# Kernel optimization log

Hardware: AMD Instinct MI355X
Metric: run time of the kernel (lower is better)

Reference implementation:

```python
import jax, jax.numpy as jnp
import numpy as np
import math

B, S, D, H = 2, 2048, 1024, 16
DK = D // H


def setup_inputs() -> dict:
    key = jax.random.key(0)
    ks = jax.random.split(key, 12)
    scale = 1.0 / math.sqrt(D)
    inp = {
        "query": jax.random.normal(ks[0], (B, S, D), jnp.float32),
        "key": jax.random.normal(ks[1], (B, S, D), jnp.float32),
        "value": jax.random.normal(ks[2], (B, S, D), jnp.float32),
        # causal 0/1 mask, broadcast over heads
        "mask": jnp.broadcast_to(jnp.tril(jnp.ones((S, S), jnp.int32)), (B, 1, S, S)),
        "Wq": jax.random.normal(ks[3], (D, D), jnp.float32) * scale,
        "bq": jnp.zeros((D,), jnp.float32),
        "Wk": jax.random.normal(ks[4], (D, D), jnp.float32) * scale,
        "bk": jnp.zeros((D,), jnp.float32),
        "Wv": jax.random.normal(ks[5], (D, D), jnp.float32) * scale,
        "bv": jnp.zeros((D,), jnp.float32),
        "Wo": jax.random.normal(ks[6], (D, D), jnp.float32) * scale,
        "bo": jnp.zeros((D,), jnp.float32),
    }
    return inp


def _split_heads(x):
    # [B,S,D] -> [B,H,S,DK]
    return x.reshape(B, S, H, DK).transpose(0, 2, 1, 3)


def reference(query, key, value, mask, Wq, bq, Wk, bk, Wv, bv, Wo, bo):
    q = _split_heads(query @ Wq.T + bq)
    k = _split_heads(key @ Wk.T + bk)
    v = _split_heads(value @ Wv.T + bv)
    # scaled dot-product attention with additive mask (mask==0 -> -inf)
    scores = jnp.einsum("bhqd,bhkd->bhqk", q, k) / math.sqrt(DK)
    scores = jnp.where(mask == 0, -jnp.inf, scores)
    w = jax.nn.softmax(scores, axis=-1)
    out = jnp.einsum("bhqk,bhkd->bhqd", w, v)
    out = out.transpose(0, 2, 1, 3).reshape(B, S, D)
    return out @ Wo.T + bo
```

## Files before the change

### kernel.cpp

```cpp
#include <hip/hip_runtime.h>
#include <hip/hip_bf16.h>
#include <math.h>

#define BBATCH 2
#define SSEQ 2048
#define DMODEL 1024
#define NH 16
#define MTOT (BBATCH*SSEQ)

typedef short bfrag __attribute__((ext_vector_type(8)));
typedef float ffrag __attribute__((ext_vector_type(4)));

typedef const __attribute__((address_space(1))) unsigned int* gas_t;
typedef __attribute__((address_space(3))) unsigned int* las_t;

__device__ __forceinline__ void dl16(const void* g, void* l) {
  __builtin_amdgcn_global_load_lds((gas_t)(unsigned long long)g,
                                   (las_t)(unsigned int)(unsigned long long)l,
                                   16, 0, 0);
}

__device__ __forceinline__ void drain_vm() {
  asm volatile("s_waitcnt vmcnt(0)" ::: "memory");
}

__device__ __forceinline__ unsigned short f2bf(float f) {
  union { float f; unsigned u; } v; v.f = f;
  unsigned r = v.u + 0x7fffu + ((v.u >> 16) & 1u);
  return (unsigned short)(r >> 16);
}

__global__ __launch_bounds__(256) void convert_all_kernel(
    const float* __restrict__ q, const float* __restrict__ k, const float* __restrict__ v,
    const float* __restrict__ wq, const float* __restrict__ wk,
    const float* __restrict__ wv, const float* __restrict__ wo,
    unsigned short* __restrict__ dst)
{
  const long NIN = (long)MTOT * DMODEL;
  const long NW  = (long)DMODEL * DMODEL;
  const long total8 = (3 * NIN + 4 * NW) >> 3;
  long i8 = (long)blockIdx.x * blockDim.x + threadIdx.x;
  const long stride = (long)gridDim.x * blockDim.x;
  for (; i8 < total8; i8 += stride) {
    const long i = i8 << 3;
    const float* src; long off;
    if (i < NIN)          { src = q; off = i; }
    else if (i < 2 * NIN) { src = k; off = i - NIN; }
    else if (i < 3 * NIN) { src = v; off = i - 2 * NIN; }
    else {
      const long j = i - 3 * NIN;
      const int wsel = (int)(j >> 20);
      off = j & (NW - 1);
      src = (wsel == 0) ? wq : (wsel == 1) ? wk : (wsel == 2) ? wv : wo;
    }
    const float4 x0 = *(const float4*)(src + off);
    const float4 x1 = *(const float4*)(src + off + 4);
    ushort4 o0, o1;
    o0.x = f2bf(x0.x); o0.y = f2bf(x0.y); o0.z = f2bf(x0.z); o0.w = f2bf(x0.w);
    o1.x = f2bf(x1.x); o1.y = f2bf(x1.y); o1.z = f2bf(x1.z); o1.w = f2bf(x1.w);
    union { ushort4 s[2]; uint4 u; } pk; pk.s[0] = o0; pk.s[1] = o1;
    *(uint4*)(dst + i) = pk.u;
  }
}

struct ProjArgs {
  const unsigned short* X[3];
  const unsigned short* W[3];
  const float* bias[3];
  unsigned short* dst[3];
  float scale[3];
};

__global__ __launch_bounds__(256, 2) void qkv_proj(ProjArgs a)
{
  __shared__ alignas(16) unsigned short As[2][128 * 64];
  __shared__ alignas(16) unsigned short Bs[2][128 * 64];
  const int t = threadIdx.x;
  const int lane = t & 63, w = t >> 6;
  const int quad = lane >> 4, l16 = lane & 15;
  const int m0 = blockIdx.x * 128;
  const int n0 = blockIdx.y * 128;
  const int z = blockIdx.z;
  const unsigned short* __restrict__ X = a.X[z];
  const unsigned short* __restrict__ W = a.W[z];
  const int wm = (w & 1) * 64, wn = (w >> 1) * 64;

  int sw[2];
#pragma unroll
  for (int c = 0; c < 2; ++c) sw[c] = (((c * 4 + quad) ^ (l16 & 7)) * 8);

  ffrag acc[4][4];
#pragma unroll
  for (int i = 0; i < 4; ++i)
#pragma unroll
    for (int j = 0; j < 4; ++j)
#pragma unroll
      for (int e = 0; e < 4; ++e) acc[i][j][e] = 0.f;

#pragma unroll
  for (int i = 0; i < 4; ++i) {
    const int ch = i * 256 + t;
    const int row = ch >> 3, lc = (ch & 7) ^ (row & 7);
    dl16(X + (size_t)(m0 + row) * DMODEL + lc * 8, As[0] + ch * 8);
    dl16(W + (size_t)(n0 + row) * DMODEL + lc * 8, Bs[0] + ch * 8);
  }

  for (int kk = 0; kk < 16; ++kk) {
    const int cur = kk & 1;
    drain_vm();
    __syncthreads();

    if (kk < 15) {
      const int k1 = (kk + 1) * 64, nxt = cur ^ 1;
#pragma unroll
      for (int i = 0; i < 4; ++i) {
        const int ch = i * 256 + t;
        const int row = ch >> 3, lc = (ch & 7) ^ (row & 7);
        dl16(X + (size_t)(m0 + row) * DMODEL + k1 + lc * 8, As[nxt] + ch * 8);
        dl16(W + (size_t)(n0 + row) * DMODEL + k1 + lc * 8, Bs[nxt] + ch * 8);
      }
    }

    bfrag af[4][2], bg[4][2];
#pragma unroll
    for (int fi = 0; fi < 4; ++fi)
#pragma unroll
      for (int c = 0; c < 2; ++c) {
        af[fi][c] = *(const bfrag*)&As[cur][(wm + fi * 16 + l16) * 64 + sw[c]];
        bg[fi][c] = *(const bfrag*)&Bs[cur][(wn + fi * 16 + l16) * 64 + sw[c]];
      }
#pragma unroll
    for (int c = 0; c < 2; ++c)
#pragma unroll
      for (int fi = 0; fi < 4; ++fi)
#pragma unroll
        for (int fj = 0; fj < 4; ++fj)
          acc[fi][fj] = __builtin_amdgcn_mfma_f32_16x16x32_bf16(af[fi][c], bg[fj][c], acc[fi][fj], 0, 0, 0);
  }

  const float sc = a.scale[z];
  const float* __restrict__ bias = a.bias[z];
  unsigned short* __restrict__ dst = a.dst[z];
#pragma unroll
  for (int fj = 0; fj < 4; ++fj) {
    const int n = n0 + wn + fj * 16 + l16;
    const float bv = bias[n];
    const int h = n >> 6, dk = n & 63;
    if (z < 2) {
#pragma unroll
      for (int fi = 0; fi < 4; ++fi)
#pragma unroll
        for (int r = 0; r < 4; ++r) {
          const int m = m0 + wm + fi * 16 + quad * 4 + r;
          const int b_ = m >> 11, s_ = m & (SSEQ - 1);
          dst[((size_t)(b_ * NH + h) * SSEQ + s_) * 64 + dk] = f2bf((acc[fi][fj][r] + bv) * sc);
        }
    } else {
#pragma unroll
      for (int fi = 0; fi < 4; ++fi) {
        const int m = m0 + wm + fi * 16 + quad * 4;
        const int b_ = m >> 11, s_ = m & (SSEQ - 1);
        ushort4 pk;
        pk.x = f2bf(acc[fi][fj][0] + bv);
        pk.y = f2bf(acc[fi][fj][1] + bv);
        pk.z = f2bf(acc[fi][fj][2] + bv);
        pk.w = f2bf(acc[fi][fj][3] + bv);
        *(ushort4*)&dst[((size_t)(b_ * NH + h) * 64 + dk) * SSEQ + s_] = pk;
      }
    }
  }
}

__global__ __launch_bounds__(256, 2) void out_proj(
    const unsigned short* __restrict__ X,
    const unsigned short* __restrict__ W,
    const float* __restrict__ bias,
    float* __restrict__ Y)
{
  __shared__ alignas(16) unsigned short As[2][128 * 64];
  __shared__ alignas(16) unsigned short Bs[2][64 * 64];
  const int t = threadIdx.x;
  const int lane = t & 63, w = t >> 6;
  const int quad = lane >> 4, l16 = lane & 15;
  const int m0 = blockIdx.x * 128;
  const int n0 = blockIdx.y * 64;
  const int wm = (w & 1) * 64, wn = (w >> 1) * 32;

  int sw[2];
#pragma unroll
  for (int c = 0; c < 2; ++c) sw[c] = (((c * 4 + quad) ^ (l16 & 7)) * 8);

  ffrag acc[4][2];
#pragma unroll
  for (int i = 0; i < 4; ++i)
#pragma unroll
    for (int j = 0; j < 2; ++j)
#pragma unroll
      for (int e = 0; e < 4; ++e) acc[i][j][e] = 0.f;

#pragma unroll
  for (int i = 0; i < 4; ++i) {
    const int ch = i * 256 + t;
    const int row = ch >> 3, lc = (ch & 7) ^ (row & 7);
    dl16(X + (size_t)(m0 + row) * DMODEL + lc * 8, As[0] + ch * 8);
  }
#pragma unroll
  for (int i = 0; i < 2; ++i) {
    const int ch = i * 256 + t;
    const int row = ch >> 3, lc = (ch & 7) ^ (row & 7);
    dl16(W + (size_t)(n0 + row) * DMODEL + lc * 8, Bs[0] + ch * 8);
  }

  for (int kk = 0; kk < 16; ++kk) {
    const int cur = kk & 1;
    drain_vm();
    __syncthreads();

    if (kk < 15) {
      const int k1 = (kk + 1) * 64, nxt = cur ^ 1;
#pragma unroll
      for (int i = 0; i < 4; ++i) {
        const int ch = i * 256 + t;
        const int row = ch >> 3, lc = (ch & 7) ^ (row & 7);
        dl16(X + (size_t)(m0 + row) * DMODEL + k1 + lc * 8, As[nxt] + ch * 8);
      }
#pragma unroll
      for (int i = 0; i < 2; ++i) {
        const int ch = i * 256 + t;
        const int row = ch >> 3, lc = (ch & 7) ^ (row & 7);
        dl16(W + (size_t)(n0 + row) * DMODEL + k1 + lc * 8, Bs[nxt] + ch * 8);
      }
    }

    bfrag af[4][2], bg[2][2];
#pragma unroll
    for (int fi = 0; fi < 4; ++fi)
#pragma unroll
      for (int c = 0; c < 2; ++c)
        af[fi][c] = *(const bfrag*)&As[cur][(wm + fi * 16 + l16) * 64 + sw[c]];
#pragma unroll
    for (int fj = 0; fj < 2; ++fj)
#pragma unroll
      for (int c = 0; c < 2; ++c)
        bg[fj][c] = *(const bfrag*)&Bs[cur][(wn + fj * 16 + l16) * 64 + sw[c]];
#pragma unroll
    for (int c = 0; c < 2; ++c)
#pragma unroll
      for (int fi = 0; fi < 4; ++fi)
#pragma unroll
        for (int fj = 0; fj < 2; ++fj)
          acc[fi][fj] = __builtin_amdgcn_mfma_f32_16x16x32_bf16(af[fi][c], bg[fj][c], acc[fi][fj], 0, 0, 0);
  }

#pragma unroll
  for (int fj = 0; fj < 2; ++fj) {
    const int n = n0 + wn + fj * 16 + l16;
    const float bv = bias[n];
#pragma unroll
    for (int fi = 0; fi < 4; ++fi)
#pragma unroll
      for (int r = 0; r < 4; ++r) {
        const int m = m0 + wm + fi * 16 + quad * 4 + r;
        Y[(size_t)m * DMODEL + n] = acc[fi][fj][r] + bv;
      }
  }
}

__global__ __launch_bounds__(256, 4) void attn_mfma(
    const unsigned short* __restrict__ Q,
    const unsigned short* __restrict__ K,
    const unsigned short* __restrict__ Vt_g,
    unsigned short* __restrict__ ctx)
{
  __shared__ alignas(16) unsigned short Kb[2][64 * 64];
  __shared__ alignas(16) unsigned short Vb[2][64 * 64];
  __shared__ alignas(16) unsigned short Pt[4][16 * 64];

  const int t = threadIdx.x;
  const int lane = t & 63, w = t >> 6;
  const int quad = lane >> 4, l16 = lane & 15;
  const int bh = blockIdx.y;
  const int qtile = blockIdx.z ? (31 - (int)blockIdx.x) : (int)blockIdx.x;
  const int i0 = qtile * 64;
  const int b_ = bh >> 4, h_ = bh & (NH - 1);
  const int q_l = w * 16 + l16;

  const unsigned short* kg = K + (size_t)bh * SSEQ * 64;
  const unsigned short* vg = Vt_g + (size_t)bh * 64 * SSEQ;

  int koff[2], voff[2], loff[2];
#pragma unroll
  for (int i = 0; i < 2; ++i) {
    const int ch = i * 256 + t;
    const int r = ch >> 3;
    const int lc = (ch & 7) ^ (r & 7);
    koff[i] = r * 64 + lc * 8;
    voff[i] = r * SSEQ + lc * 8;
    loff[i] = ch * 8;
  }
  int sw[2];
#pragma unroll
  for (int c = 0; c < 2; ++c) sw[c] = (((c * 4 + quad) ^ (l16 & 7)) * 8);
  const int pwr = l16 * 64 + (quad & 1) * 4;

#pragma unroll
  for (int i = 0; i < 2; ++i) {
    dl16(kg + koff[i], Kb[0] + loff[i]);
    dl16(vg + voff[i], Vb[0] + loff[i]);
  }

  const unsigned short* qg = Q + ((size_t)bh * SSEQ + i0) * 64;
  bfrag qb[2];
#pragma unroll
  for (int c = 0; c < 2; ++c)
    qb[c] = *(const bfrag*)(qg + (size_t)q_l * 64 + c * 32 + quad * 8);

  bfrag onesf;
#pragma unroll
  for (int j = 0; j < 8; ++j) onesf[j] = (short)0x3F80;

  ffrag o[4], lacc;
#pragma unroll
  for (int fn = 0; fn < 4; ++fn)
#pragma unroll
    for (int e = 0; e < 4; ++e) o[fn][e] = 0.f;
#pragma unroll
  for (int e = 0; e < 4; ++e) lacc[e] = 0.f;

  for (int jt = 0; jt < qtile + 1; ++jt) {
    const int cur = jt & 1;
    const bool diag = (jt == qtile);
    drain_vm();
    __syncthreads();

    if (!diag) {
      const int nxt = cur ^ 1;
#pragma unroll
      for (int i = 0; i < 2; ++i) {
        dl16(kg + (size_t)(jt + 1) * 4096 + koff[i], Kb[nxt] + loff[i]);
        dl16(vg + (size_t)(jt + 1) * 64   + voff[i], Vb[nxt] + loff[i]);
      }
    }

    ffrag s[4];
#pragma unroll
    for (int fj = 0; fj < 4; ++fj)
#pragma unroll
      for (int e = 0; e < 4; ++e) s[fj][e] = 0.f;
#pragma unroll
    for (int c = 0; c < 2; ++c)
#pragma unroll
      for (int fj = 0; fj < 4; ++fj) {
        bfrag ka = *(const bfrag*)&Kb[cur][(fj * 16 + l16) * 64 + sw[c]];
        s[fj] = __builtin_amdgcn_mfma_f32_16x16x32_bf16(ka, qb[c], s[fj], 0, 0, 0);
      }

    if (diag) {
#pragma unroll
      for (int fj = 0; fj < 4; ++fj) {
        float p[4];
#pragma unroll
        for (int r = 0; r < 4; ++r) {
          const float pe = exp2f(s[fj][r]);
          p[r] = ((fj * 16 + quad * 4 + r) > q_l) ? 0.f : pe;
        }
        float2 lo; lo.x = p[0]; lo.y = p[1];
        float2 hi; hi.x = p[2]; hi.y = p[3];
        union { __hip_bfloat162 h[2]; unsigned long long u; } cv;
        cv.h[0] = __float22bfloat162_rn(lo);
        cv.h[1] = __float22bfloat162_rn(hi);
        const int cc = fj * 2 + (quad >> 1);
        *(unsigned long long*)&Pt[w][pwr + ((cc ^ (l16 & 7)) * 8)] = cv.u;
      }
    } else {
#pragma unroll
      for (int fj = 0; fj < 4; ++fj) {
        float2 lo; lo.x = exp2f(s[fj][0]); lo.y = exp2f(s[fj][1]);
        float2 hi; hi.x = exp2f(s[fj][2]); hi.y = exp2f(s[fj][3]);
        union { __hip_bfloat162 h[2]; unsigned long long u; } cv;
        cv.h[0] = __float22bfloat162_rn(lo);
        cv.h[1] = __float22bfloat162_rn(hi);
        const int cc = fj * 2 + (quad >> 1);
        *(unsigned long long*)&Pt[w][pwr + ((cc ^ (l16 & 7)) * 8)] = cv.u;
      }
    }
    asm volatile("s_waitcnt lgkmcnt(0)" ::: "memory");

#pragma unroll
    for (int c = 0; c < 2; ++c) {
      bfrag pb = *(const bfrag*)&Pt[w][l16 * 64 + sw[c]];
      lacc = __builtin_amdgcn_mfma_f32_16x16x32_bf16(onesf, pb, lacc, 0, 0, 0);
#pragma unroll
      for (int fn = 0; fn < 4; ++fn) {
        bfrag va = *(const bfrag*)&Vb[cur][(fn * 16 + l16) * 64 + sw[c]];
        o[fn] = __builtin_amdgcn_mfma_f32_16x16x32_bf16(va, pb, o[fn], 0, 0, 0);
      }
    }
  }

  const float inv = 1.f / lacc[0];
  unsigned short* cbase = ctx + (size_t)(b_ * SSEQ + i0 + q_l) * DMODEL + h_ * 64;
#pragma unroll
  for (int fn = 0; fn < 4; ++fn) {
    float2 lo; lo.x = o[fn][0] * inv; lo.y = o[fn][1] * inv;
    float2 hi; hi.x = o[fn][2] * inv; hi.y = o[fn][3] * inv;
    union { __hip_bfloat162 h[2]; unsigned long long u; } cv;
    cv.h[0] = __float22bfloat162_rn(lo);
    cv.h[1] = __float22bfloat162_rn(hi);
    *(unsigned long long*)(cbase + fn * 16 + quad * 4) = cv.u;
  }
}

extern "C" void kernel_launch(void* const* d_in, const int* in_sizes, int n_in,
                              void* d_out, int out_size, void* d_ws, size_t ws_size,
                              hipStream_t stream)
{
  const float* q  = (const float*)d_in[0];
  const float* k  = (const float*)d_in[1];
  const float* v  = (const float*)d_in[2];
  const float* wq = (const float*)d_in[4];
  const float* bq = (const float*)d_in[5];
  const float* wk = (const float*)d_in[6];
  const float* bk = (const float*)d_in[7];
  const float* wv = (const float*)d_in[8];
  const float* bv = (const float*)d_in[9];
  const float* wo = (const float*)d_in[10];
  const float* bo = (const float*)d_in[11];

  const long NIN = (long)MTOT * DMODEL;
  const long NW  = (long)DMODEL * DMODEL;
  unsigned short* ws16 = (unsigned short*)d_ws;
  unsigned short* qx  = ws16;
  unsigned short* kx  = qx + NIN;
  unsigned short* vx  = kx + NIN;
  unsigned short* wqb = vx + NIN;
  unsigned short* wkb = wqb + NW;
  unsigned short* wvb = wkb + NW;
  unsigned short* wob = wvb + NW;
  unsigned short* Qp  = wob + NW;
  unsigned short* Kp  = Qp + NIN;
  unsigned short* Vp  = Kp + NIN;
  unsigned short* Cx  = Vp + NIN;

  convert_all_kernel<<<2048, 256, 0, stream>>>(q, k, v, wq, wk, wv, wo, ws16);

  ProjArgs pa;
  pa.X[0] = qx;  pa.X[1] = kx;  pa.X[2] = vx;
  pa.W[0] = wqb; pa.W[1] = wkb; pa.W[2] = wvb;
  pa.bias[0] = bq; pa.bias[1] = bk; pa.bias[2] = bv;
  pa.dst[0] = Qp; pa.dst[1] = Kp; pa.dst[2] = Vp;
  pa.scale[0] = 0.18033688011112042f;
  pa.scale[1] = 1.0f;
  pa.scale[2] = 1.0f;
  qkv_proj<<<dim3(MTOT / 128, DMODEL / 128, 3), 256, 0, stream>>>(pa);

  attn_mfma<<<dim3(16, BBATCH * NH, 2), 256, 0, stream>>>(Qp, Kp, Vp, Cx);

  out_proj<<<dim3(MTOT / 128, DMODEL / 64), 256, 0, stream>>>(Cx, wob, bo, (float*)d_out);
}
```

Measured before the change: 226.6 us.

## Fuse fp32-to-bf16 activation conversion into QKV projection A-loads, use native exp2

Stops pre-converting the query/key/value activations to bf16 in a separate pass. The QKV projection now reads fp32 activations straight from global memory into registers and converts them on the fly, dropping the A-tile LDS staging. This removes one full read/write round trip of three 4M-element tensors. The cost is that A-operand loads are now synchronous per-thread global loads with no double buffering, and each activation tile is re-read by every N-block. The attention softmax also switches to the hardware exp2 builtin.

```diff
diff --git a/kernel.cpp b/kernel.cpp
--- a/kernel.cpp
+++ b/kernel.cpp
@@ -24,35 +24,47 @@
   asm volatile("s_waitcnt vmcnt(0)" ::: "memory");
 }
 
+#if defined(__has_builtin) && __has_builtin(__builtin_amdgcn_exp2f)
+__device__ __forceinline__ float fexp2(float x) { return __builtin_amdgcn_exp2f(x); }
+#else
+__device__ __forceinline__ float fexp2(float x) { return exp2f(x); }
+#endif
+
 __device__ __forceinline__ unsigned short f2bf(float f) {
   union { float f; unsigned u; } v; v.f = f;
   unsigned r = v.u + 0x7fffu + ((v.u >> 16) & 1u);
   return (unsigned short)(r >> 16);
 }
 
-__global__ __launch_bounds__(256) void convert_all_kernel(
-    const float* __restrict__ q, const float* __restrict__ k, const float* __restrict__ v,
+__device__ __forceinline__ bfrag load_a_bf16(const float* p) {
+  const float4 x0 = *(const float4*)p;
+  const float4 x1 = *(const float4*)(p + 4);
+  union { __hip_bfloat162 h[4]; bfrag f; } u;
+  float2 t0; t0.x = x0.x; t0.y = x0.y;
+  float2 t1; t1.x = x0.z; t1.y = x0.w;
+  float2 t2; t2.x = x1.x; t2.y = x1.y;
+  float2 t3; t3.x = x1.z; t3.y = x1.w;
+  u.h[0] = __float22bfloat162_rn(t0);
+  u.h[1] = __float22bfloat162_rn(t1);
+  u.h[2] = __float22bfloat162_rn(t2);
+  u.h[3] = __float22bfloat162_rn(t3);
+  return u.f;
+}
+
+__global__ __launch_bounds__(256) void convert_w_kernel(
     const float* __restrict__ wq, const float* __restrict__ wk,
     const float* __restrict__ wv, const float* __restrict__ wo,
     unsigned short* __restrict__ dst)
 {
-  const long NIN = (long)MTOT * DMODEL;
-  const long NW  = (long)DMODEL * DMODEL;
-  const long total8 = (3 * NIN + 4 * NW) >> 3;
+  const long NW = (long)DMODEL * DMODEL;
+  const long total8 = (4 * NW) >> 3;
   long i8 = (long)blockIdx.x * blockDim.x + threadIdx.x;
   const long stride = (long)gridDim.x * blockDim.x;
   for (; i8 < total8; i8 += stride) {
     const long i = i8 << 3;
-    const float* src; long off;
-    if (i < NIN)          { src = q; off = i; }
-    else if (i < 2 * NIN) { src = k; off = i - NIN; }
-    else if (i < 3 * NIN) { src = v; off = i - 2 * NIN; }
-    else {
-      const long j = i - 3 * NIN;
-      const int wsel = (int)(j >> 20);
-      off = j & (NW - 1);
-      src = (wsel == 0) ? wq : (wsel == 1) ? wk : (wsel == 2) ? wv : wo;
-    }
+    const int wsel = (int)(i >> 20);
+    const long off = i & (NW - 1);
+    const float* src = (wsel == 0) ? wq : (wsel == 1) ? wk : (wsel == 2) ? wv : wo;
     const float4 x0 = *(const float4*)(src + off);
     const float4 x1 = *(const float4*)(src + off + 4);
     ushort4 o0, o1;
@@ -64,7 +76,7 @@
 }
 
 struct ProjArgs {
-  const unsigned short* X[3];
+  const float* X[3];
   const unsigned short* W[3];
   const float* bias[3];
   unsigned short* dst[3];
@@ -73,7 +85,6 @@
 
 __global__ __launch_bounds__(256, 2) void qkv_proj(ProjArgs a)
 {
-  __shared__ alignas(16) unsigned short As[2][128 * 64];
   __shared__ alignas(16) unsigned short Bs[2][128 * 64];
   const int t = threadIdx.x;
   const int lane = t & 63, w = t >> 6;
@@ -81,13 +92,18 @@
   const int m0 = blockIdx.x * 128;
   const int n0 = blockIdx.y * 128;
   const int z = blockIdx.z;
-  const unsigned short* __restrict__ X = a.X[z];
+  const float* __restrict__ X = a.X[z];
   const unsigned short* __restrict__ W = a.W[z];
   const int wm = (w & 1) * 64, wn = (w >> 1) * 64;
 
   int sw[2];
 #pragma unroll
   for (int c = 0; c < 2; ++c) sw[c] = (((c * 4 + quad) ^ (l16 & 7)) * 8);
+
+  const float* xrow[4];
+#pragma unroll
+  for (int fi = 0; fi < 4; ++fi)
+    xrow[fi] = X + (size_t)(m0 + wm + fi * 16 + l16) * DMODEL + quad * 8;
 
   ffrag acc[4][4];
 #pragma unroll
@@ -101,22 +117,21 @@
   for (int i = 0; i < 4; ++i) {
     const int ch = i * 256 + t;
     const int row = ch >> 3, lc = (ch & 7) ^ (row & 7);
-    dl16(X + (size_t)(m0 + row) * DMODEL + lc * 8, As[0] + ch * 8);
     dl16(W + (size_t)(n0 + row) * DMODEL + lc * 8, Bs[0] + ch * 8);
   }
 
   for (int kk = 0; kk < 16; ++kk) {
     const int cur = kk & 1;
+    const int k0 = kk * 64;
     drain_vm();
     __syncthreads();
 
     if (kk < 15) {
-      const int k1 = (kk + 1) * 64, nxt = cur ^ 1;
+      const int k1 = k0 + 64, nxt = cur ^ 1;
 #pragma unroll
       for (int i = 0; i < 4; ++i) {
         const int ch = i * 256 + t;
         const int row = ch >> 3, lc = (ch & 7) ^ (row & 7);
-        dl16(X + (size_t)(m0 + row) * DMODEL + k1 + lc * 8, As[nxt] + ch * 8);
         dl16(W + (size_t)(n0 + row) * DMODEL + k1 + lc * 8, Bs[nxt] + ch * 8);
       }
     }
@@ -125,10 +140,13 @@
 #pragma unroll
     for (int fi = 0; fi < 4; ++fi)
 #pragma unroll
-      for (int c = 0; c < 2; ++c) {
-        af[fi][c] = *(const bfrag*)&As[cur][(wm + fi * 16 + l16) * 64 + sw[c]];
+      for (int c = 0; c < 2; ++c)
+        af[fi][c] = load_a_bf16(xrow[fi] + k0 + c * 32);
+#pragma unroll
+    for (int fi = 0; fi < 4; ++fi)
+#pragma unroll
+      for (int c = 0; c < 2; ++c)
         bg[fi][c] = *(const bfrag*)&Bs[cur][(wn + fi * 16 + l16) * 64 + sw[c]];
-      }
 #pragma unroll
     for (int c = 0; c < 2; ++c)
 #pragma unroll
@@ -361,7 +379,7 @@
         float p[4];
 #pragma unroll
         for (int r = 0; r < 4; ++r) {
-          const float pe = exp2f(s[fj][r]);
+          const float pe = fexp2(s[fj][r]);
           p[r] = ((fj * 16 + quad * 4 + r) > q_l) ? 0.f : pe;
         }
         float2 lo; lo.x = p[0]; lo.y = p[1];
@@ -375,8 +393,8 @@
     } else {
 #pragma unroll
       for (int fj = 0; fj < 4; ++fj) {
-        float2 lo; lo.x = exp2f(s[fj][0]); lo.y = exp2f(s[fj][1]);
-        float2 hi; hi.x = exp2f(s[fj][2]); hi.y = exp2f(s[fj][3]);
+        float2 lo; lo.x = fexp2(s[fj][0]); lo.y = fexp2(s[fj][1]);
+        float2 hi; hi.x = fexp2(s[fj][2]); hi.y = fexp2(s[fj][3]);
         union { __hip_bfloat162 h[2]; unsigned long long u; } cv;
         cv.h[0] = __float22bfloat162_rn(lo);
         cv.h[1] = __float22bfloat162_rn(hi);
@@ -430,10 +448,7 @@
   const long NIN = (long)MTOT * DMODEL;
   const long NW  = (long)DMODEL * DMODEL;
   unsigned short* ws16 = (unsigned short*)d_ws;
-  unsigned short* qx  = ws16;
-  unsigned short* kx  = qx + NIN;
-  unsigned short* vx  = kx + NIN;
-  unsigned short* wqb = vx + NIN;
+  unsigned short* wqb = ws16;
   unsigned short* wkb = wqb + NW;
   unsigned short* wvb = wkb + NW;
   unsigned short* wob = wvb + NW;
@@ -442,10 +457,10 @@
   unsigned short* Vp  = Kp + NIN;
   unsigned short* Cx  = Vp + NIN;
 
-  convert_all_kernel<<<2048, 256, 0, stream>>>(q, k, v, wq, wk, wv, wo, ws16);
+  convert_w_kernel<<<1024, 256, 0, stream>>>(wq, wk, wv, wo, ws16);
 
   ProjArgs pa;
-  pa.X[0] = qx;  pa.X[1] = kx;  pa.X[2] = vx;
+  pa.X[0] = q;   pa.X[1] = k;   pa.X[2] = v;
   pa.W[0] = wqb; pa.W[1] = wkb; pa.W[2] = wvb;
   pa.bias[0] = bq; pa.bias[1] = bk; pa.bias[2] = bv;
   pa.dst[0] = Qp; pa.dst[1] = Kp; pa.dst[2] = Vp;
```

Result: slower. 283.3 us (+25.0%).
